# Performance work log

Measured on AMD Instinct MI355X. Metric: run time of the kernel, lower is better.

## Reference

```python
import jax, jax.numpy as jnp
import numpy as np

WD, WH, WW = 1, 8, 8           # window size
NH = 2                          # num heads
EPS = 1e-5                      # torch LayerNorm default


def _layernorm(x, g, b):
    mu = jnp.mean(x, axis=-1, keepdims=True)
    var = jnp.mean((x - mu) ** 2, axis=-1, keepdims=True)
    return (x - mu) * jax.lax.rsqrt(var + EPS) * g + b


def setup_inputs() -> dict:
    key = jax.random.key(0)
    ks = jax.random.split(key, 12)
    C, H = 192, 768  # dim, mlp hidden
    w = lambda k, shape: (jax.random.normal(k, shape, jnp.float32) * 0.02)
    return {
        "x": jax.random.normal(ks[0], (2, 8, 96, 96, C), jnp.float32),
        "norm3_g": jnp.ones((C,), jnp.float32),
        "norm3_b": jnp.zeros((C,), jnp.float32),
        "in_proj_w": w(ks[1], (3 * C, C)),
        "in_proj_b": jnp.zeros((3 * C,), jnp.float32),
        "out_proj_w": w(ks[2], (C, C)),
        "out_proj_b": jnp.zeros((C,), jnp.float32),
        "norm4_g": jnp.ones((C,), jnp.float32),
        "norm4_b": jnp.zeros((C,), jnp.float32),
        "fc1_w": w(ks[3], (H, C)),
        "fc1_b": jnp.zeros((H,), jnp.float32),
        "fc2_w": w(ks[4], (C, H)),
        "fc2_b": jnp.zeros((C,), jnp.float32),
    }


def _part3(x, norm3_g, norm3_b, in_proj_w, in_proj_b, out_proj_w, out_proj_b):
    B, D, H, W, C = x.shape
    Dn, Hn, Wn = D // WD, H // WH, W // WW
    P = Hn * Wn          # spatial windows
    Wt = WD * WH * WW    # tokens per window (64)
    L = Dn * Wt          # attention sequence length

    xn = _layernorm(x, norm3_g, norm3_b)
    # window partition: (B, Dn, Hn, Wn, wd, wh, ww, C)
    xw = xn.reshape(B, Dn, WD, Hn, WH, Wn, WW, C).transpose(0, 1, 3, 5, 2, 4, 6, 7)
    # tgt: (B, Dn, P, Wt, C) -> h: (B*P, Dn*Wt, C)
    tgt = xw.reshape(B, Dn, P, Wt, C)
    h = tgt.transpose(0, 2, 1, 3, 4).reshape(B * P, L, C)

    # qkv projection (torch Linear convention: x @ W.T + b)
    qkv = h @ in_proj_w.T + in_proj_b          # (Bp, L, 3C)
    q, k, v = jnp.split(qkv, 3, axis=-1)
    hd = C // NH
    q = q.reshape(B * P, L, NH, hd)
    k = k.reshape(B * P, L, NH, hd)
    v = v.reshape(B * P, L, NH, hd)

    # block-causal mask over temporal index (each block is Wt x Wt)
    neg_inf = jnp.finfo(jnp.float32).min
    tmask = jnp.triu(jnp.full((Dn, Dn), neg_inf, jnp.float32), k=1)
    mask = jnp.repeat(jnp.repeat(tmask, Wt, axis=0), Wt, axis=1)  # (L, L)

    scale = 1.0 / np.sqrt(hd)
    scores = jnp.einsum("blhd,bmhd->bhlm", q * scale, k) + mask
    attn = jax.nn.softmax(scores, axis=-1)
    out = jnp.einsum("bhlm,bmhd->blhd", attn, v).reshape(B * P, L, C)
    out = out @ out_proj_w.T + out_proj_b

    # reverse: (B, P, Dn, Wt, C) -> windows -> (B, D, H, W, C)
    out = out.reshape(B, P, Dn, Wt, C).transpose(0, 2, 1, 3, 4)
    out = out.reshape(B, Dn, Hn, Wn, WD, WH, WW, C)
    out = out.transpose(0, 1, 4, 2, 5, 3, 6, 7).reshape(B, D, H, W, C)
    return out


def reference(x, norm3_g, norm3_b, in_proj_w, in_proj_b, out_proj_w, out_proj_b,
              norm4_g, norm4_b, fc1_w, fc1_b, fc2_w, fc2_b):
    x = x + _part3(x, norm3_g, norm3_b, in_proj_w, in_proj_b, out_proj_w, out_proj_b)
    xn = _layernorm(x, norm4_g, norm4_b)
    mlp = jax.nn.gelu(xn @ fc1_w.T + fc1_b, approximate=False) @ fc2_w.T + fc2_b
    return x + mlp
```

## Files before the change

### kernel.cpp

```cpp
#include <hip/hip_runtime.h>
#include <cstdint>
#include <cstddef>


typedef float   f32x4  __attribute__((ext_vector_type(4)));
typedef __bf16  bf16x8 __attribute__((ext_vector_type(8)));
typedef unsigned int   u32x4  __attribute__((ext_vector_type(4)));
typedef unsigned short u16x4  __attribute__((ext_vector_type(4)));

#define DEVI __device__ __forceinline__

DEVI float bf2f(unsigned short u) {
    union { unsigned int i; float f; } v; v.i = ((unsigned int)u) << 16; return v.f;
}
DEVI unsigned short f2bf(float f) {
    unsigned int u = __builtin_bit_cast(unsigned int, f);
    unsigned int r = u + 0x7fffu + ((u >> 16) & 1u);
    return (unsigned short)(r >> 16);
}

typedef __attribute__((address_space(3))) unsigned char       lds_u8;
typedef __attribute__((address_space(1))) const unsigned char g_u8;
DEVI void gl_lds16(const void* g, void* l) {
    __builtin_amdgcn_global_load_lds((g_u8*)g, (lds_u8*)l, 16, 0, 0);
}

__global__ __launch_bounds__(256) void k_wconv(const float* __restrict__ wqkv,
                                               const float* __restrict__ wout,
                                               const float* __restrict__ wfc1,
                                               const float* __restrict__ wfc2,
                                               unsigned short* __restrict__ oq,
                                               unsigned short* __restrict__ oo,
                                               unsigned short* __restrict__ o1,
                                               unsigned short* __restrict__ o2) {
    int i = blockIdx.x * 256 + threadIdx.x;
    if (i < 122880) {
        int r = i / 192;
        oq[i] = (r < 576) ? f2bf(wqkv[i]) : (unsigned short)0;
    } else if (i < 172032) {
        int j = i - 122880; int r = j / 192;
        oo[j] = (r < 192) ? f2bf(wout[j]) : (unsigned short)0;
    } else if (i < 319488) {
        int j = i - 172032;
        o1[j] = f2bf(wfc1[j]);
    } else if (i < 516096) {
        int j = i - 319488; int r = j / 768;
        o2[j] = (r < 192) ? f2bf(wfc2[j]) : (unsigned short)0;
    }
}

__global__ __launch_bounds__(256) void k_ln3(const float* __restrict__ x,
                                             const float* __restrict__ g,
                                             const float* __restrict__ bsh,
                                             unsigned short* __restrict__ h) {
    int w = threadIdx.x >> 6, lane = threadIdx.x & 63;
    int token = blockIdx.x * 4 + w;
    const float* xp = x + (size_t)token * 192;
    float v0 = xp[lane], v1 = xp[lane + 64], v2 = xp[lane + 128];
    float s = v0 + v1 + v2;
#pragma unroll
    for (int off = 32; off; off >>= 1) s += __shfl_xor(s, off);
    float mean = s * (1.f / 192.f);
    float d0 = v0 - mean, d1 = v1 - mean, d2 = v2 - mean;
    float q = d0 * d0 + d1 * d1 + d2 * d2;
#pragma unroll
    for (int off = 32; off; off >>= 1) q += __shfl_xor(q, off);
    float rs = rsqrtf(q * (1.f / 192.f) + 1e-5f);
    int b  = token / (8 * 96 * 96);
    int r0 = token - b * (8 * 96 * 96);
    int d  = r0 / (96 * 96);
    int r1 = r0 - d * (96 * 96);
    int hh = r1 / 96;
    int ww = r1 - hh * 96;
    int bp = b * 144 + (hh >> 3) * 12 + (ww >> 3);
    int l  = d * 64 + (hh & 7) * 8 + (ww & 7);
    unsigned short* hp = h + ((size_t)bp * 512 + l) * 192;
    hp[lane]       = f2bf(d0 * rs * g[lane]       + bsh[lane]);
    hp[lane + 64]  = f2bf(d1 * rs * g[lane + 64]  + bsh[lane + 64]);
    hp[lane + 128] = f2bf(d2 * rs * g[lane + 128] + bsh[lane + 128]);
}

__global__ __launch_bounds__(256) void k_ln4(const float* __restrict__ yv,
                                             const float* __restrict__ g,
                                             const float* __restrict__ bsh,
                                             unsigned short* __restrict__ xn) {
    int w = threadIdx.x >> 6, lane = threadIdx.x & 63;
    size_t token = (size_t)blockIdx.x * 4 + w;
    const float* xp = yv + token * 192;
    float v0 = xp[lane], v1 = xp[lane + 64], v2 = xp[lane + 128];
    float s = v0 + v1 + v2;
#pragma unroll
    for (int off = 32; off; off >>= 1) s += __shfl_xor(s, off);
    float mean = s * (1.f / 192.f);
    float d0 = v0 - mean, d1 = v1 - mean, d2 = v2 - mean;
    float q = d0 * d0 + d1 * d1 + d2 * d2;
#pragma unroll
    for (int off = 32; off; off >>= 1) q += __shfl_xor(q, off);
    float rs = rsqrtf(q * (1.f / 192.f) + 1e-5f);
    unsigned short* op = xn + token * 192;
    op[lane]       = f2bf(d0 * rs * g[lane]       + bsh[lane]);
    op[lane + 64]  = f2bf(d1 * rs * g[lane + 64]  + bsh[lane + 64]);
    op[lane + 128] = f2bf(d2 * rs * g[lane + 128] + bsh[lane + 128]);
}

template <int EPI, int K>
__global__ __launch_bounds__(256) void k_gemm128(const unsigned short* __restrict__ A,
                                                 const unsigned short* __restrict__ Bw,
                                                 const float* __restrict__ bias,
                                                 unsigned short* __restrict__ outb,
                                                 unsigned short* __restrict__ vt,
                                                 float* __restrict__ outf,
                                                 const float* __restrict__ res) {
    __shared__ unsigned short As[128 * 64];
    __shared__ unsigned short Bs[128 * 64];
    const int tid = threadIdx.x;
    const int nwg = gridDim.x * gridDim.y;
    const int flat = blockIdx.y * gridDim.x + blockIdx.x;
    const int swz = (flat & 7) * (nwg >> 3) + (flat >> 3);
    const int bx = swz % gridDim.x, by = swz / gridDim.x;
    const int row0 = by * 128, col0 = bx * 128;
    const int wv = tid >> 6, lane = tid & 63, lr = lane & 15, lg = lane >> 4;
    const int wr = wv >> 1, wc = wv & 1;
    const int sr = lane >> 3, sc = lane & 7;
    f32x4 acc[4][4] = {};

    for (int k0 = 0; k0 < K; k0 += 64) {
#pragma unroll
        for (int i = 0; i < 4; i++) {
            int g = wv * 4 + i;
            int r = g * 8 + sr;
            int j = sc ^ (r & 7);
            gl_lds16(A + (size_t)(row0 + r) * K + k0 + j * 8, &As[g * 512]);
        }
#pragma unroll
        for (int i = 0; i < 4; i++) {
            int g = wv * 4 + i;
            int r = g * 8 + sr;
            int j = sc ^ (r & 7);
            gl_lds16(Bw + (size_t)(col0 + r) * K + k0 + j * 8, &Bs[g * 512]);
        }
        __syncthreads();
#pragma unroll
        for (int kk = 0; kk < 64; kk += 32) {
            bf16x8 af[4], bf[4];
#pragma unroll
            for (int m = 0; m < 4; m++) {
                int r = wr * 64 + m * 16 + lr;
                int j = ((kk >> 3) + lg) ^ (r & 7);
                af[m] = __builtin_bit_cast(bf16x8,
                    *reinterpret_cast<const u32x4*>(&As[r * 64 + j * 8]));
            }
#pragma unroll
            for (int n = 0; n < 4; n++) {
                int r = wc * 64 + n * 16 + lr;
                int j = ((kk >> 3) + lg) ^ (r & 7);
                bf[n] = __builtin_bit_cast(bf16x8,
                    *reinterpret_cast<const u32x4*>(&Bs[r * 64 + j * 8]));
            }
#pragma unroll
            for (int m = 0; m < 4; m++)
#pragma unroll
                for (int n = 0; n < 4; n++)
                    acc[m][n] = __builtin_amdgcn_mfma_f32_16x16x32_bf16(af[m], bf[n], acc[m][n], 0, 0, 0);
        }
        __syncthreads();
    }

#pragma unroll
    for (int m = 0; m < 4; m++) {
#pragma unroll
        for (int n = 0; n < 4; n++) {
            int col  = col0 + wc * 64 + n * 16 + lr;
            int rowb = row0 + wr * 64 + m * 16 + lg * 4;
            if constexpr (EPI == 0) {
                if (col < 384) {
                    float b = bias[col];
                    float sc2 = (col < 192) ? 0.1020620726159658f : 1.f;
#pragma unroll
                    for (int rr = 0; rr < 4; rr++)
                        outb[(size_t)(rowb + rr) * 384 + col] = f2bf((acc[m][n][rr] + b) * sc2);
                } else if (col < 576) {
                    float b = bias[col];
                    int head = (col >= 480) ? 1 : 0;
                    int d = col - 384 - head * 96;
                    int bp = rowb >> 9, tok = rowb & 511;
                    u16x4 pk = { f2bf(acc[m][n][0] + b), f2bf(acc[m][n][1] + b),
                                 f2bf(acc[m][n][2] + b), f2bf(acc[m][n][3] + b) };
                    *reinterpret_cast<u16x4*>(vt + ((size_t)(bp * 2 + head) * 96 + d) * 512 + tok) = pk;
                }
            } else if constexpr (EPI == 1) {
                if (col < 192) {
                    float b = bias[col];
#pragma unroll
                    for (int rr = 0; rr < 4; rr++) {
                        int nrow = rowb + rr;
                        int bp = nrow >> 9, l = nrow & 511;
                        int bb = bp / 144, p = bp - bb * 144;
                        int hn = p / 12, wn = p - hn * 12;
                        int dn = l >> 6, t_ = l & 63;
                        size_t tok = ((size_t)((bb * 8 + dn) * 96 + hn * 8 + (t_ >> 3)) * 96 + wn * 8 + (t_ & 7));
                        size_t idx = tok * 192 + col;
                        outf[idx] = res[idx] + acc[m][n][rr] + b;
                    }
                }
            } else if constexpr (EPI == 2) {
                float b = bias[col];
#pragma unroll
                for (int rr = 0; rr < 4; rr++) {
                    float v = acc[m][n][rr] + b;
                    float gz = 0.5f * v * (1.f + erff(v * 0.70710678118654752f));
                    outb[(size_t)(rowb + rr) * 768 + col] = f2bf(gz);
                }
            } else {
                if (col < 192) {
                    float b = bias[col];
#pragma unroll
                    for (int rr = 0; rr < 4; rr++) {
                        size_t idx = (size_t)(rowb + rr) * 192 + col;
                        outf[idx] = res[idx] + acc[m][n][rr] + b;
                    }
                }
            }
        }
    }
}

__global__ __launch_bounds__(512) void k_attn(const unsigned short* __restrict__ qk,
                                              const unsigned short* __restrict__ vt,
                                              unsigned short* __restrict__ aout) {
    __shared__ unsigned short Ks[64][104];
    __shared__ unsigned short Vs[96][72];
    __shared__ unsigned short Ps[8][16][72];

    int bid = (blockIdx.x & 7) * 288 + (blockIdx.x >> 3);
    int bp = bid >> 3, rest = bid & 7, head = rest >> 2, pr = rest & 3;
    int tid = threadIdx.x, wv = tid >> 6, lane = tid & 63;
    int lr = lane & 15, lg = lane >> 4;
    int wq = wv & 3, wt = wv >> 2;
    int nk = 2 * pr + 2;

    size_t qrow0 = (size_t)bp * 512 + (size_t)(2 * pr + wt) * 64;
    const unsigned short* vbase = vt + (size_t)(bp * 2 + head) * 96 * 512;
    size_t krowb = (size_t)bp * 512;

    bf16x8 qf[3];
    {
        const unsigned short* qp = qk + (qrow0 + wq * 16 + lr) * 384 + head * 96 + lg * 8;
#pragma unroll
        for (int ks = 0; ks < 3; ks++)
            qf[ks] = __builtin_bit_cast(bf16x8, *reinterpret_cast<const u32x4*>(qp + ks * 32));
    }

    f32x4 o[6] = {};
    float m_ = -1e30f, lsum = 0.f;

    u32x4 sreg[3];
    auto issue = [&](int dnk) {
#pragma unroll
        for (int i = 0; i < 3; i++) {
            int c = tid + i * 512;
            if (c < 768) {
                int r = c / 12, cc = c - r * 12;
                sreg[i] = *reinterpret_cast<const u32x4*>(
                    qk + (krowb + dnk * 64 + r) * 384 + 192 + head * 96 + cc * 8);
            } else {
                int c2 = c - 768; int d = c2 >> 3, tb = c2 & 7;
                sreg[i] = *reinterpret_cast<const u32x4*>(
                    vbase + (size_t)d * 512 + dnk * 64 + tb * 8);
            }
        }
    };
    auto commit = [&]() {
#pragma unroll
        for (int i = 0; i < 3; i++) {
            int c = tid + i * 512;
            if (c < 768) {
                int r = c / 12, cc = c - r * 12;
                *reinterpret_cast<u32x4*>(&Ks[r][cc * 8]) = sreg[i];
            } else {
                int c2 = c - 768; int d = c2 >> 3, tb = c2 & 7;
                *reinterpret_cast<u32x4*>(&Vs[d][tb * 8]) = sreg[i];
            }
        }
    };

    issue(0);
    for (int dnk = 0; dnk < nk; ++dnk) {
        commit();
        __syncthreads();
        if (dnk + 1 < nk) issue(dnk + 1);
        if (wt == 1 || dnk < nk - 1) {
            f32x4 st[4] = {};
#pragma unroll
            for (int ks = 0; ks < 3; ks++) {
#pragma unroll
                for (int ct = 0; ct < 4; ct++) {
                    bf16x8 kf = __builtin_bit_cast(bf16x8,
                        *reinterpret_cast<const u32x4*>(&Ks[ct * 16 + lr][ks * 32 + lg * 8]));
                    st[ct] = __builtin_amdgcn_mfma_f32_16x16x32_bf16(kf, qf[ks], st[ct], 0, 0, 0);
                }
            }
            float mx = st[0][0];
#pragma unroll
            for (int ct = 0; ct < 4; ct++)
#pragma unroll
                for (int rr = 0; rr < 4; rr++) mx = fmaxf(mx, st[ct][rr]);
            mx = fmaxf(mx, __shfl_xor(mx, 16));
            mx = fmaxf(mx, __shfl_xor(mx, 32));
            float mnew = fmaxf(m_, mx);
            float corr = __expf(m_ - mnew);
            m_ = mnew;
            float ps = 0.f;
#pragma unroll
            for (int ct = 0; ct < 4; ct++) {
                u16x4 pk;
#pragma unroll
                for (int rr = 0; rr < 4; rr++) {
                    float pv = __expf(st[ct][rr] - mnew);
                    ps += pv;
                    pk[rr] = f2bf(pv);
                }
                *reinterpret_cast<u16x4*>(&Ps[wv][lr][ct * 16 + lg * 4]) = pk;
            }
            ps += __shfl_xor(ps, 16);
            ps += __shfl_xor(ps, 32);
            lsum = lsum * corr + ps;
#pragma unroll
            for (int rr = 0; rr < 4; rr++) {
                float cr = __shfl(corr, (lane & 48) | (lg * 4 + rr));
#pragma unroll
                for (int nf = 0; nf < 6; nf++) o[nf][rr] *= cr;
            }
#pragma unroll
            for (int kk = 0; kk < 2; kk++) {
                bf16x8 pf = __builtin_bit_cast(bf16x8,
                    *reinterpret_cast<const u32x4*>(&Ps[wv][lr][kk * 32 + lg * 8]));
#pragma unroll
                for (int nf = 0; nf < 6; nf++) {
                    bf16x8 vf = __builtin_bit_cast(bf16x8,
                        *reinterpret_cast<const u32x4*>(&Vs[nf * 16 + lr][kk * 32 + lg * 8]));
                    o[nf] = __builtin_amdgcn_mfma_f32_16x16x32_bf16(pf, vf, o[nf], 0, 0, 0);
                }
            }
        }
        __syncthreads();
    }

#pragma unroll
    for (int rr = 0; rr < 4; rr++) {
        float li = __shfl(lsum, (lane & 48) | (lg * 4 + rr));
        float inv = 1.f / li;
        size_t row = qrow0 + wq * 16 + lg * 4 + rr;
#pragma unroll
        for (int nf = 0; nf < 6; nf++)
            aout[row * 192 + head * 96 + nf * 16 + lr] = f2bf(o[nf][rr] * inv);
    }
}

extern "C" void kernel_launch(void* const* d_in, const int* in_sizes, int n_in,
                              void* d_out, int out_size, void* d_ws, size_t ws_size,
                              hipStream_t stream) {
    const float* x    = (const float*)d_in[0];
    const float* n3g  = (const float*)d_in[1];
    const float* n3b  = (const float*)d_in[2];
    const float* wqkv = (const float*)d_in[3];
    const float* bqkv = (const float*)d_in[4];
    const float* wout = (const float*)d_in[5];
    const float* bout = (const float*)d_in[6];
    const float* n4g  = (const float*)d_in[7];
    const float* n4b  = (const float*)d_in[8];
    const float* wfc1 = (const float*)d_in[9];
    const float* bfc1 = (const float*)d_in[10];
    const float* wfc2 = (const float*)d_in[11];
    const float* bfc2 = (const float*)d_in[12];
    float* out = (float*)d_out;

    char* ws = (char*)d_ws;
    unsigned short* qk     = (unsigned short*)(ws + 0);
    unsigned short* vt     = (unsigned short*)(ws + 113246208);
    unsigned short* h      = (unsigned short*)(ws + 169869312);
    unsigned short* attn   = (unsigned short*)(ws + 226492416);
    unsigned short* xn4    = (unsigned short*)(ws + 226492416);
    unsigned short* hidden = (unsigned short*)(ws + 0);
    unsigned short* wq_bf  = (unsigned short*)(ws + 283115520);
    unsigned short* wo_bf  = (unsigned short*)(ws + 283361280);
    unsigned short* w1_bf  = (unsigned short*)(ws + 283459584);
    unsigned short* w2_bf  = (unsigned short*)(ws + 283754496);
    float* y = out;

    k_wconv<<<2016, 256, 0, stream>>>(wqkv, wout, wfc1, wfc2, wq_bf, wo_bf, w1_bf, w2_bf);
    k_ln3<<<36864, 256, 0, stream>>>(x, n3g, n3b, h);
    k_gemm128<0, 192><<<dim3(5, 1152), 256, 0, stream>>>(h, wq_bf, bqkv, qk, vt, nullptr, nullptr);
    k_attn<<<2304, 512, 0, stream>>>(qk, vt, attn);
    k_gemm128<1, 192><<<dim3(2, 1152), 256, 0, stream>>>(attn, wo_bf, bout, nullptr, nullptr, y, x);
    k_ln4<<<36864, 256, 0, stream>>>(y, n4g, n4b, xn4);
    k_gemm128<2, 192><<<dim3(6, 1152), 256, 0, stream>>>(xn4, w1_bf, bfc1, hidden, nullptr, nullptr, nullptr);
    k_gemm128<3, 768><<<dim3(2, 1152), 256, 0, stream>>>(hidden, w2_bf, bfc2, nullptr, nullptr, out, y);
}
```

Baseline: 605.6 us.

## Store post-attention residual in bf16 and double-buffer GEMM LDS tiles

```diff
diff --git a/kernel.cpp b/kernel.cpp
--- a/kernel.cpp
+++ b/kernel.cpp
@@ -80,27 +80,38 @@
     hp[lane + 128] = f2bf(d2 * rs * g[lane + 128] + bsh[lane + 128]);
 }
 
-__global__ __launch_bounds__(256) void k_ln4(const float* __restrict__ yv,
-                                             const float* __restrict__ g,
-                                             const float* __restrict__ bsh,
-                                             unsigned short* __restrict__ xn) {
-    int w = threadIdx.x >> 6, lane = threadIdx.x & 63;
-    size_t token = (size_t)blockIdx.x * 4 + w;
-    const float* xp = yv + token * 192;
-    float v0 = xp[lane], v1 = xp[lane + 64], v2 = xp[lane + 128];
-    float s = v0 + v1 + v2;
-#pragma unroll
-    for (int off = 32; off; off >>= 1) s += __shfl_xor(s, off);
+__global__ __launch_bounds__(256) void k_ln4b(const unsigned short* __restrict__ yb,
+                                              const float* __restrict__ g,
+                                              const float* __restrict__ bsh,
+                                              unsigned short* __restrict__ xn) {
+    int sub = threadIdx.x >> 5, tl = threadIdx.x & 31;
+    size_t row = (size_t)blockIdx.x * 8 + sub;
+    const unsigned int* rp = reinterpret_cast<const unsigned int*>(yb + row * 192);
+    float v[6];
+#pragma unroll
+    for (int j = 0; j < 3; j++) {
+        unsigned int w = rp[tl + 32 * j];
+        v[2 * j]     = bf2f((unsigned short)(w & 0xffffu));
+        v[2 * j + 1] = bf2f((unsigned short)(w >> 16));
+    }
+    float s = v[0] + v[1] + v[2] + v[3] + v[4] + v[5];
+#pragma unroll
+    for (int off = 1; off < 32; off <<= 1) s += __shfl_xor(s, off);
     float mean = s * (1.f / 192.f);
-    float d0 = v0 - mean, d1 = v1 - mean, d2 = v2 - mean;
-    float q = d0 * d0 + d1 * d1 + d2 * d2;
-#pragma unroll
-    for (int off = 32; off; off >>= 1) q += __shfl_xor(q, off);
+    float q = 0.f;
+#pragma unroll
+    for (int j = 0; j < 6; j++) { v[j] -= mean; q += v[j] * v[j]; }
+#pragma unroll
+    for (int off = 1; off < 32; off <<= 1) q += __shfl_xor(q, off);
     float rs = rsqrtf(q * (1.f / 192.f) + 1e-5f);
-    unsigned short* op = xn + token * 192;
-    op[lane]       = f2bf(d0 * rs * g[lane]       + bsh[lane]);
-    op[lane + 64]  = f2bf(d1 * rs * g[lane + 64]  + bsh[lane + 64]);
-    op[lane + 128] = f2bf(d2 * rs * g[lane + 128] + bsh[lane + 128]);
+    unsigned int* op = reinterpret_cast<unsigned int*>(xn + row * 192);
+#pragma unroll
+    for (int j = 0; j < 3; j++) {
+        int c = (tl + 32 * j) * 2;
+        unsigned short lo = f2bf(v[2 * j]     * rs * g[c]     + bsh[c]);
+        unsigned short hi = f2bf(v[2 * j + 1] * rs * g[c + 1] + bsh[c + 1]);
+        op[tl + 32 * j] = ((unsigned int)hi << 16) | lo;
+    }
 }
 
 template <int EPI, int K>
@@ -110,9 +121,10 @@
                                                  unsigned short* __restrict__ outb,
                                                  unsigned short* __restrict__ vt,
                                                  float* __restrict__ outf,
-                                                 const float* __restrict__ res) {
-    __shared__ unsigned short As[128 * 64];
-    __shared__ unsigned short Bs[128 * 64];
+                                                 const float* __restrict__ res,
+                                                 const unsigned short* __restrict__ resb) {
+    __shared__ unsigned short As[2][128 * 64];
+    __shared__ unsigned short Bs[2][128 * 64];
     const int tid = threadIdx.x;
     const int nwg = gridDim.x * gridDim.y;
     const int flat = blockIdx.y * gridDim.x + blockIdx.x;
@@ -124,22 +136,30 @@
     const int sr = lane >> 3, sc = lane & 7;
     f32x4 acc[4][4] = {};
 
-    for (int k0 = 0; k0 < K; k0 += 64) {
+    auto stage = [&](int t, int buf) {
+        int k0 = t * 64;
 #pragma unroll
         for (int i = 0; i < 4; i++) {
-            int g = wv * 4 + i;
-            int r = g * 8 + sr;
+            int gq = wv * 4 + i;
+            int r = gq * 8 + sr;
             int j = sc ^ (r & 7);
-            gl_lds16(A + (size_t)(row0 + r) * K + k0 + j * 8, &As[g * 512]);
+            gl_lds16(A + (size_t)(row0 + r) * K + k0 + j * 8, &As[buf][gq * 512]);
         }
 #pragma unroll
         for (int i = 0; i < 4; i++) {
-            int g = wv * 4 + i;
-            int r = g * 8 + sr;
+            int gq = wv * 4 + i;
+            int r = gq * 8 + sr;
             int j = sc ^ (r & 7);
-            gl_lds16(Bw + (size_t)(col0 + r) * K + k0 + j * 8, &Bs[g * 512]);
-        }
-        __syncthreads();
+            gl_lds16(Bw + (size_t)(col0 + r) * K + k0 + j * 8, &Bs[buf][gq * 512]);
+        }
+    };
+
+    const int NT = K / 64;
+    stage(0, 0);
+    __syncthreads();
+    for (int t = 0; t < NT; ++t) {
+        int cur = t & 1;
+        if (t + 1 < NT) stage(t + 1, cur ^ 1);
 #pragma unroll
         for (int kk = 0; kk < 64; kk += 32) {
             bf16x8 af[4], bf[4];
@@ -148,14 +168,14 @@
                 int r = wr * 64 + m * 16 + lr;
                 int j = ((kk >> 3) + lg) ^ (r & 7);
                 af[m] = __builtin_bit_cast(bf16x8,
-                    *reinterpret_cast<const u32x4*>(&As[r * 64 + j * 8]));
+                    *reinterpret_cast<const u32x4*>(&As[cur][r * 64 + j * 8]));
             }
 #pragma unroll
             for (int n = 0; n < 4; n++) {
                 int r = wc * 64 + n * 16 + lr;
                 int j = ((kk >> 3) + lg) ^ (r & 7);
                 bf[n] = __builtin_bit_cast(bf16x8,
-                    *reinterpret_cast<const u32x4*>(&Bs[r * 64 + j * 8]));
+                    *reinterpret_cast<const u32x4*>(&Bs[cur][r * 64 + j * 8]));
             }
 #pragma unroll
             for (int m = 0; m < 4; m++)
@@ -200,7 +220,7 @@
                         int dn = l >> 6, t_ = l & 63;
                         size_t tok = ((size_t)((bb * 8 + dn) * 96 + hn * 8 + (t_ >> 3)) * 96 + wn * 8 + (t_ & 7));
                         size_t idx = tok * 192 + col;
-                        outf[idx] = res[idx] + acc[m][n][rr] + b;
+                        outb[idx] = f2bf(res[idx] + acc[m][n][rr] + b);
                     }
                 }
             } else if constexpr (EPI == 2) {
@@ -217,7 +237,7 @@
 #pragma unroll
                     for (int rr = 0; rr < 4; rr++) {
                         size_t idx = (size_t)(rowb + rr) * 192 + col;
-                        outf[idx] = res[idx] + acc[m][n][rr] + b;
+                        outf[idx] = bf2f(resb[idx]) + acc[m][n][rr] + b;
                     }
                 }
             }
@@ -386,14 +406,14 @@
     unsigned short* wo_bf  = (unsigned short*)(ws + 283361280);
     unsigned short* w1_bf  = (unsigned short*)(ws + 283459584);
     unsigned short* w2_bf  = (unsigned short*)(ws + 283754496);
-    float* y = out;
+    unsigned short* ybf    = (unsigned short*)(ws + 284147712);
 
     k_wconv<<<2016, 256, 0, stream>>>(wqkv, wout, wfc1, wfc2, wq_bf, wo_bf, w1_bf, w2_bf);
     k_ln3<<<36864, 256, 0, stream>>>(x, n3g, n3b, h);
-    k_gemm128<0, 192><<<dim3(5, 1152), 256, 0, stream>>>(h, wq_bf, bqkv, qk, vt, nullptr, nullptr);
+    k_gemm128<0, 192><<<dim3(5, 1152), 256, 0, stream>>>(h, wq_bf, bqkv, qk, vt, nullptr, nullptr, nullptr);
     k_attn<<<2304, 512, 0, stream>>>(qk, vt, attn);
-    k_gemm128<1, 192><<<dim3(2, 1152), 256, 0, stream>>>(attn, wo_bf, bout, nullptr, nullptr, y, x);
-    k_ln4<<<36864, 256, 0, stream>>>(y, n4g, n4b, xn4);
-    k_gemm128<2, 192><<<dim3(6, 1152), 256, 0, stream>>>(xn4, w1_bf, bfc1, hidden, nullptr, nullptr, nullptr);
-    k_gemm128<3, 768><<<dim3(2, 1152), 256, 0, stream>>>(hidden, w2_bf, bfc2, nullptr, nullptr, out, y);
-}
+    k_gemm128<1, 192><<<dim3(2, 1152), 256, 0, stream>>>(attn, wo_bf, bout, ybf, nullptr, nullptr, x, nullptr);
+    k_ln4b<<<18432, 256, 0, stream>>>(ybf, n4g, n4b, xn4);
+    k_gemm128<2, 192><<<dim3(6, 1152), 256, 0, stream>>>(xn4, w1_bf, bfc1, hidden, nullptr, nullptr, nullptr, nullptr);
+    k_gemm128<3, 768><<<dim3(2, 1152), 256, 0, stream>>>(hidden, w2_bf, bfc2, nullptr, nullptr, out, nullptr, ybf);
+}
```

New measurement: 611.3 us. About the same (+0.9%).
